# Kernel tuning notes

Measured on AMD Instinct MI355X. Metric: run time of the kernel, lower is better.

The kernel has to match this reference:

```python
import jax, jax.numpy as jnp
import numpy as np

B, T, D, H = 4, 2048, 1024, 16
HD = D // H  # head_size = 64
EPS = 1e-5


def layernorm(x, g, b):
    mu = jnp.mean(x, axis=-1, keepdims=True)
    var = jnp.var(x, axis=-1, keepdims=True)
    return (x - mu) * jax.lax.rsqrt(var + EPS) * g + b


def setup_inputs() -> dict:
    key = jax.random.key(0)
    ks = jax.random.split(key, 8)
    s = 0.02
    return {
        "x": jax.random.normal(ks[0], (B, T, D), jnp.float32),
        "Wq": jax.random.normal(ks[1], (D, D), jnp.float32) * s,
        "Wk": jax.random.normal(ks[2], (D, D), jnp.float32) * s,
        "Wv": jax.random.normal(ks[3], (D, D), jnp.float32) * s,
        "Wo": jax.random.normal(ks[4], (D, D), jnp.float32) * s,
        "bo": jnp.zeros((D,), jnp.float32),
        "W1": jax.random.normal(ks[5], (D, 4 * D), jnp.float32) * s,
        "b1": jnp.zeros((4 * D,), jnp.float32),
        "W2": jax.random.normal(ks[6], (4 * D, D), jnp.float32) * s,
        "b2": jnp.zeros((D,), jnp.float32),
        "ln1_g": jnp.ones((D,), jnp.float32),
        "ln1_b": jnp.zeros((D,), jnp.float32),
        "ln2_g": jnp.ones((D,), jnp.float32),
        "ln2_b": jnp.zeros((D,), jnp.float32),
    }


def reference(x, Wq, Wk, Wv, Wo, bo, W1, b1, W2, b2, ln1_g, ln1_b, ln2_g, ln2_b):
    # --- multi-head causal self-attention (pre-LN), dropout off (eval) ---
    h = layernorm(x, ln1_g, ln1_b)
    q = jnp.einsum('btd,de->bte', h, Wq).reshape(B, T, H, HD)
    k = jnp.einsum('btd,de->bte', h, Wk).reshape(B, T, H, HD)
    v = jnp.einsum('btd,de->bte', h, Wv).reshape(B, T, H, HD)
    scores = jnp.einsum('bqhd,bkhd->bhqk', q, k) * (HD ** -0.5)
    causal = jnp.tril(jnp.ones((T, T), bool))
    scores = jnp.where(causal, scores, -jnp.inf)
    attn = jax.nn.softmax(scores, axis=-1)
    out = jnp.einsum('bhqk,bkhd->bqhd', attn, v).reshape(B, T, D)
    out = jnp.einsum('btd,de->bte', out, Wo) + bo
    x = x + out
    # --- feed-forward: Linear -> ReLU -> Linear -> ReLU (as in source) ---
    h2 = layernorm(x, ln2_g, ln2_b)
    ff = jax.nn.relu(jnp.einsum('btd,df->btf', h2, W1) + b1)
    ff = jax.nn.relu(jnp.einsum('btf,fd->btd', ff, W2) + b2)
    return x + ff
```

## Files before the change

### kernel.cpp

```cpp
#include <hip/hip_runtime.h>
#include <cstdint>
#include <cstddef>

typedef unsigned short u16;
typedef __attribute__((ext_vector_type(8))) short bf16x8;
typedef __attribute__((ext_vector_type(4))) float f32x4;
typedef __attribute__((address_space(1))) const unsigned int gu32;
typedef __attribute__((address_space(3))) unsigned int lu32;

#define QSCALE 0.1803368801111204f

__device__ __forceinline__ u16 f2bf(float f) {
  uint32_t u = __float_as_uint(f);
  u += 0x7fffu + ((u >> 16) & 1u);
  return (u16)(u >> 16);
}

__device__ __forceinline__ void xcd_swz(int& bn, int& bm) {
  int gx = (int)gridDim.x;
  int n = gx * (int)gridDim.y;
  int lid = (int)blockIdx.x + gx * (int)blockIdx.y;
  int nid = (lid & 7) * (n >> 3) + (lid >> 3);
  bn = nid % gx;
  bm = nid / gx;
}

__global__ __launch_bounds__(256) void transpose_w(const float* __restrict__ W,
                                                   u16* __restrict__ WT,
                                                   int K, int N) {
  __shared__ float t[32][33];
  int n0 = blockIdx.x * 32, k0 = blockIdx.y * 32;
  for (int i = threadIdx.y; i < 32; i += 8)
    t[i][threadIdx.x] = W[(size_t)(k0 + i) * N + n0 + threadIdx.x];
  __syncthreads();
  for (int i = threadIdx.y; i < 32; i += 8)
    WT[(size_t)(n0 + i) * K + k0 + threadIdx.x] = f2bf(t[threadIdx.x][i]);
}

__global__ __launch_bounds__(256) void transpose_w4(
    const float* __restrict__ W0, const float* __restrict__ W1,
    const float* __restrict__ W2, const float* __restrict__ W3,
    u16* __restrict__ D0, u16* __restrict__ D1,
    u16* __restrict__ D2, u16* __restrict__ D3) {
  __shared__ float t[32][33];
  const float* W = (blockIdx.z == 0) ? W0 : (blockIdx.z == 1) ? W1
                   : (blockIdx.z == 2) ? W2 : W3;
  u16* D = (blockIdx.z == 0) ? D0 : (blockIdx.z == 1) ? D1
           : (blockIdx.z == 2) ? D2 : D3;
  int n0 = blockIdx.x * 32, k0 = blockIdx.y * 32;
  for (int i = threadIdx.y; i < 32; i += 8)
    t[i][threadIdx.x] = W[(size_t)(k0 + i) * 1024 + n0 + threadIdx.x];
  __syncthreads();
  for (int i = threadIdx.y; i < 32; i += 8)
    D[(size_t)(n0 + i) * 1024 + k0 + threadIdx.x] = f2bf(t[threadIdx.x][i]);
}

__global__ __launch_bounds__(256) void ln_kernel(const float* __restrict__ x,
                                                 const float* __restrict__ g,
                                                 const float* __restrict__ b,
                                                 u16* __restrict__ out) {
  int row = blockIdx.x;
  const float4 v = *(const float4*)(x + (size_t)row * 1024 + threadIdx.x * 4);
  float s = v.x + v.y + v.z + v.w;
  float ss = v.x * v.x + v.y * v.y + v.z * v.z + v.w * v.w;
#pragma unroll
  for (int d = 1; d < 64; d <<= 1) { s += __shfl_xor(s, d); ss += __shfl_xor(ss, d); }
  __shared__ float rs_[4], rss_[4];
  int wv = threadIdx.x >> 6;
  if ((threadIdx.x & 63) == 0) { rs_[wv] = s; rss_[wv] = ss; }
  __syncthreads();
  s = rs_[0] + rs_[1] + rs_[2] + rs_[3];
  ss = rss_[0] + rss_[1] + rss_[2] + rss_[3];
  float mu = s * (1.f / 1024.f);
  float var = ss * (1.f / 1024.f) - mu * mu;
  float rstd = rsqrtf(var + 1e-5f);
  float4 gv = *(const float4*)(g + threadIdx.x * 4);
  float4 bv = *(const float4*)(b + threadIdx.x * 4);
  uint32_t lo = (uint32_t)f2bf((v.x - mu) * rstd * gv.x + bv.x) |
                ((uint32_t)f2bf((v.y - mu) * rstd * gv.y + bv.y) << 16);
  uint32_t hi = (uint32_t)f2bf((v.z - mu) * rstd * gv.z + bv.z) |
                ((uint32_t)f2bf((v.w - mu) * rstd * gv.w + bv.w) << 16);
  uint2 o; o.x = lo; o.y = hi;
  *(uint2*)(out + (size_t)row * 1024 + threadIdx.x * 4) = o;
}

#define G128A(is)                                                             \
  __builtin_amdgcn_global_load_lds(                                           \
      (gu32*)((const char*)(A + (size_t)(bm * 128 + (is) * 32 + srow) * K +   \
                            (size_t)kt * 64) + ssw),                          \
      (lu32*)&lds[(is) * 2048 + wid * 512], 16, 0, 0)
#define G128B(is)                                                             \
  __builtin_amdgcn_global_load_lds(                                           \
      (gu32*)((const char*)(BT + (size_t)(bn * 128 + (is) * 32 + srow) * K +  \
                            (size_t)kt * 64) + ssw),                          \
      (lu32*)&lds[8192 + (is) * 2048 + wid * 512], 16, 0, 0)

template <int MODE>
__global__ __launch_bounds__(256, 4) void g128(
    const u16* __restrict__ A, const u16* __restrict__ BT,
    int M, int N, int K,
    const float* __restrict__ bias, const float* __restrict__ resid,
    float* __restrict__ outf,
    u16* __restrict__ ob0, u16* __restrict__ ob1, u16* __restrict__ ob2) {
  __shared__ __align__(16) u16 lds[16384];
  const int tid = threadIdx.x, lane = tid & 63, wid = tid >> 6;
  const int wr = wid >> 1, wc = wid & 1;
  int bn, bm;
  xcd_swz(bn, bm);
  const int l15 = lane & 15, lhi = lane >> 4;
  const int srow = tid >> 3;
  const int ssw = ((tid & 7) * 16) ^ ((srow & 7) << 4);
  const int swz = (l15 & 7) << 4;
  const int cb0 = (lhi * 16) ^ swz;
  const int cb1 = (64 + lhi * 16) ^ swz;
  const char* Ab = (const char*)lds;
  const char* Bb = (const char*)lds + 16384;

  f32x4 acc[4][4];
#pragma unroll
  for (int i = 0; i < 4; ++i)
#pragma unroll
    for (int j = 0; j < 4; ++j) acc[i][j] = (f32x4){0.f, 0.f, 0.f, 0.f};

  const int NT = K >> 6;

  for (int kt = 0; kt < NT; ++kt) {
    __syncthreads();
    G128A(0); G128A(1); G128A(2); G128A(3);
    G128B(0); G128B(1); G128B(2); G128B(3);
    __syncthreads();
#pragma unroll
    for (int ks = 0; ks < 2; ++ks) {
      const int cb = ks ? cb1 : cb0;
      bf16x8 af[4], bf[4];
#pragma unroll
      for (int mi = 0; mi < 4; ++mi)
        af[mi] = *(const bf16x8*)(Ab + (wr * 64 + mi * 16 + l15) * 128 + cb);
#pragma unroll
      for (int ni = 0; ni < 4; ++ni)
        bf[ni] = *(const bf16x8*)(Bb + (wc * 64 + ni * 16 + l15) * 128 + cb);
#pragma unroll
      for (int mi = 0; mi < 4; ++mi)
#pragma unroll
        for (int ni = 0; ni < 4; ++ni)
          acc[mi][ni] = __builtin_amdgcn_mfma_f32_16x16x32_bf16(af[mi], bf[ni], acc[mi][ni], 0, 0, 0);
    }
  }

  char* ep = (char*)lds;
  if (MODE == 0 && bn >= 16) {
#pragma unroll
    for (int h = 0; h < 2; ++h) {
      __syncthreads();
      if (wc == h) {
#pragma unroll
        for (int mi = 0; mi < 4; ++mi)
#pragma unroll
          for (int ni = 0; ni < 4; ++ni) {
            uint32_t lo, hi;
            asm("v_cvt_pk_bf16_f32 %0, %1, %2"
                : "=v"(lo) : "v"(acc[mi][ni][0]), "v"(acc[mi][ni][1]));
            asm("v_cvt_pk_bf16_f32 %0, %1, %2"
                : "=v"(hi) : "v"(acc[mi][ni][2]), "v"(acc[mi][ni][3]));
            uint2 pk; pk.x = lo; pk.y = hi;
            int c_local = ni * 16 + l15;
            int rb = wr * 64 + mi * 16 + lhi * 4;
            *(uint2*)(ep + c_local * 264 + rb * 2) = pk;
          }
      }
      __syncthreads();
#pragma unroll
      for (int it = 0; it < 4; ++it) {
        int idx = it * 256 + tid;
        int c = idx >> 4, tc = idx & 15;
        uint4 d4 = *(const uint4*)(ep + c * 264 + tc * 16);
        int cm = bn * 128 + h * 64 + c - 2048, hh = cm >> 6, dd = cm & 63;
        size_t bh = (size_t)((bm >> 4) * 16 + hh);
        int t0 = (bm & 15) * 128;
        *(uint4*)&ob2[(bh * 64 + dd) * 2048 + t0 + tc * 8] = d4;
      }
    }
  } else if (MODE == 0 || MODE == 2) {
    const float sc = (MODE == 0 && bn < 8) ? QSCALE : 1.f;
#pragma unroll
    for (int h = 0; h < 2; ++h) {
      __syncthreads();
      if (wr == h) {
#pragma unroll
        for (int mi = 0; mi < 4; ++mi)
#pragma unroll
          for (int ni = 0; ni < 4; ++ni) {
            int c_local = wc * 64 + ni * 16 + l15;
            int rb = mi * 16 + lhi * 4;
            float bv = (MODE == 2) ? bias[bn * 128 + c_local] : 0.f;
#pragma unroll
            for (int r = 0; r < 4; ++r) {
              float v = acc[mi][ni][r];
              v = (MODE == 2) ? fmaxf(v + bv, 0.f) : v * sc;
              *(u16*)(ep + (rb + r) * 272 + c_local * 2) = f2bf(v);
            }
          }
      }
      __syncthreads();
#pragma unroll
      for (int it = 0; it < 4; ++it) {
        int idx = it * 256 + tid;
        int row = idx >> 4, cc = idx & 15;
        uint4 d4 = *(const uint4*)(ep + row * 272 + cc * 16);
        size_t rg = (size_t)(bm * 128 + h * 64 + row);
        int colg = bn * 128 + cc * 8;
        if (MODE == 2) {
          *(uint4*)&ob0[rg * (size_t)N + colg] = d4;
        } else if (colg < 1024) {
          *(uint4*)&ob0[rg * 1024 + colg] = d4;
        } else {
          *(uint4*)&ob1[rg * 1024 + colg - 1024] = d4;
        }
      }
    }
  } else {
    float* epf = (float*)lds;
#pragma unroll
    for (int q = 0; q < 4; ++q) {
      __syncthreads();
      if (wr == (q >> 1)) {
#pragma unroll
        for (int mh = 0; mh < 2; ++mh) {
          int mi = (q & 1) * 2 + mh;
#pragma unroll
          for (int ni = 0; ni < 4; ++ni) {
            int c_local = wc * 64 + ni * 16 + l15;
            int rl = mh * 16 + lhi * 4;
#pragma unroll
            for (int r = 0; r < 4; ++r)
              epf[(rl + r) * 132 + c_local] = acc[mi][ni][r];
          }
        }
      }
      __syncthreads();
#pragma unroll
      for (int it = 0; it < 4; ++it) {
        int idx = it * 256 + tid;
        int row = idx >> 5, cc = idx & 31;
        float4 v = *(const float4*)&epf[row * 132 + cc * 4];
        int colg = bn * 128 + cc * 4;
        size_t rg = (size_t)(bm * 128 + q * 32 + row);
        float4 bv = *(const float4*)&bias[colg];
        float4 rv = *(const float4*)&resid[rg * (size_t)N + colg];
        float4 o4;
        if (MODE == 1) {
          o4.x = v.x + bv.x + rv.x; o4.y = v.y + bv.y + rv.y;
          o4.z = v.z + bv.z + rv.z; o4.w = v.w + bv.w + rv.w;
        } else {
          o4.x = fmaxf(v.x + bv.x, 0.f) + rv.x;
          o4.y = fmaxf(v.y + bv.y, 0.f) + rv.y;
          o4.z = fmaxf(v.z + bv.z, 0.f) + rv.z;
          o4.w = fmaxf(v.w + bv.w, 0.f) + rv.w;
        }
        *(float4*)&outf[rg * (size_t)N + colg] = o4;
      }
    }
  }
}

__global__ __launch_bounds__(512) void attn_kernel(
    const u16* __restrict__ Qb, const u16* __restrict__ Kb,
    const u16* __restrict__ VTb, u16* __restrict__ O) {
  const int lid = (int)blockIdx.x + 8 * (int)blockIdx.y;
  const int p = (lid >> 3) & 7;
  const int bh = ((lid >> 6) << 3) | (lid & 7);
  const int b = bh >> 4, h = bh & 15;
  const u16* Q = Qb + (size_t)b * 2048 * 1024 + h * 64;
  const u16* Kn = Kb + (size_t)b * 2048 * 1024 + h * 64;
  const u16* VT = VTb + (size_t)bh * 64 * 2048;
  const int tid = threadIdx.x, lane = tid & 63, wv = tid >> 6;
  const int l15 = lane & 15, lhi = lane >> 4;
  const int srow = tid >> 3;
  const int scol16 = (tid & 7) * 16;
  const int sw = scol16 ^ ((srow & 7) << 4);
  const int rswz = (l15 & 7) << 4;
  const int cb0 = (lhi * 16) ^ rswz;
  const int cb1 = (64 + lhi * 16) ^ rswz;

  __shared__ __align__(16) u16 KV[3][2][4096];
  __shared__ u16 Ps[8][16 * 72];

  bf16x8 onesf;
#pragma unroll
  for (int i = 0; i < 8; ++i) onesf[i] = (short)0x3F80;

#define STAGEKV(slot, kt)                                                     \
  do {                                                                        \
    __builtin_amdgcn_global_load_lds(                                         \
        (gu32*)((const char*)(Kn + (size_t)((kt)*64 + srow) * 1024) + sw),    \
        (lu32*)&KV[slot][0][wv * 512], 16, 0, 0);                             \
    __builtin_amdgcn_global_load_lds(                                         \
        (gu32*)((const char*)(VT + (size_t)srow * 2048 + (kt)*64) + sw),      \
        (lu32*)&KV[slot][1][wv * 512], 16, 0, 0);                             \
  } while (0)

#pragma unroll
  for (int pass = 0; pass < 2; ++pass) {
    const int chunk = pass ? p : (15 - p);
    const int qbase = chunk * 128 + wv * 16;
    const int nkt = 2 * chunk + 2;

    bf16x8 qf[2];
#pragma unroll
    for (int ks = 0; ks < 2; ++ks)
      qf[ks] = *(const bf16x8*)&Q[(size_t)(qbase + l15) * 1024 + ks * 32 + lhi * 8];

    f32x4 o[4];
#pragma unroll
    for (int f = 0; f < 4; ++f) o[f] = (f32x4){0.f, 0.f, 0.f, 0.f};
    f32x4 lacc = (f32x4){0.f, 0.f, 0.f, 0.f};

    __syncthreads();
    STAGEKV(0, 0);
    STAGEKV(1, 1);

    for (int kt = 0; kt < nkt; ++kt) {
      if (kt + 1 < nkt) {
        asm volatile("s_waitcnt vmcnt(2)" ::: "memory");
      } else {
        asm volatile("s_waitcnt vmcnt(0)" ::: "memory");
      }
      __syncthreads();

      const int cs = kt % 3;
      if (kt * 64 <= qbase + 15) {
        const char* Kbase = (const char*)&KV[cs][0][0];
        const char* Vbase = (const char*)&KV[cs][1][0];

        f32x4 s[4];
#pragma unroll
        for (int jt = 0; jt < 4; ++jt) s[jt] = (f32x4){0.f, 0.f, 0.f, 0.f};
        __builtin_amdgcn_s_setprio(1);
#pragma unroll
        for (int ks = 0; ks < 2; ++ks) {
          const int cbyte = ks ? cb1 : cb0;
#pragma unroll
          for (int jt = 0; jt < 4; ++jt) {
            bf16x8 kf = *(const bf16x8*)(Kbase + (jt * 16 + l15) * 128 + cbyte);
            s[jt] = __builtin_amdgcn_mfma_f32_16x16x32_bf16(kf, qf[ks], s[jt], 0, 0, 0);
          }
        }
        __builtin_amdgcn_s_setprio(0);

        if (kt * 64 + 63 > qbase) {
          int qg = qbase + l15;
#pragma unroll
          for (int jt = 0; jt < 4; ++jt)
#pragma unroll
            for (int r = 0; r < 4; ++r) {
              int kg = kt * 64 + jt * 16 + lhi * 4 + r;
              if (kg > qg) s[jt][r] = -1e30f;
            }
        }

#pragma unroll
        for (int jt = 0; jt < 4; ++jt)
#pragma unroll
          for (int r = 0; r < 4; ++r) s[jt][r] = exp2f(s[jt][r]);

#pragma unroll
        for (int jt = 0; jt < 4; ++jt) {
          uint32_t lo, hi;
          asm("v_cvt_pk_bf16_f32 %0, %1, %2"
              : "=v"(lo) : "v"(s[jt][0]), "v"(s[jt][1]));
          asm("v_cvt_pk_bf16_f32 %0, %1, %2"
              : "=v"(hi) : "v"(s[jt][2]), "v"(s[jt][3]));
          uint2 pk; pk.x = lo; pk.y = hi;
          *(uint2*)&Ps[wv][l15 * 72 + jt * 16 + lhi * 4] = pk;
        }
        __builtin_amdgcn_s_setprio(1);
#pragma unroll
        for (int ks = 0; ks < 2; ++ks) {
          const int cbyte = ks ? cb1 : cb0;
          bf16x8 pf = *(const bf16x8*)&Ps[wv][l15 * 72 + ks * 32 + lhi * 8];
          lacc = __builtin_amdgcn_mfma_f32_16x16x32_bf16(pf, onesf, lacc, 0, 0, 0);
#pragma unroll
          for (int f = 0; f < 4; ++f) {
            bf16x8 vfr = *(const bf16x8*)(Vbase + (f * 16 + l15) * 128 + cbyte);
            o[f] = __builtin_amdgcn_mfma_f32_16x16x32_bf16(pf, vfr, o[f], 0, 0, 0);
          }
        }
        __builtin_amdgcn_s_setprio(0);
      }

      if (kt + 2 < nkt) STAGEKV((kt + 2) % 3, kt + 2);
    }

#pragma unroll
    for (int r = 0; r < 4; ++r) {
      float inv = 1.f / lacc[r];
      int t = qbase + lhi * 4 + r;
#pragma unroll
      for (int f = 0; f < 4; ++f)
        O[((size_t)(b * 2048 + t)) * 1024 + h * 64 + f * 16 + l15] = f2bf(o[f][r] * inv);
    }
  }
#undef STAGEKV
}

extern "C" void kernel_launch(void* const* d_in, const int* in_sizes, int n_in,
                              void* d_out, int out_size, void* d_ws, size_t ws_size,
                              hipStream_t stream) {
  const float* x   = (const float*)d_in[0];
  const float* Wq  = (const float*)d_in[1];
  const float* Wk  = (const float*)d_in[2];
  const float* Wv  = (const float*)d_in[3];
  const float* Wo  = (const float*)d_in[4];
  const float* bo  = (const float*)d_in[5];
  const float* W1  = (const float*)d_in[6];
  const float* b1  = (const float*)d_in[7];
  const float* W2  = (const float*)d_in[8];
  const float* b2  = (const float*)d_in[9];
  const float* g1  = (const float*)d_in[10];
  const float* be1 = (const float*)d_in[11];
  const float* g2  = (const float*)d_in[12];
  const float* be2 = (const float*)d_in[13];

  char* p = (char*)d_ws;
  auto alloc = [&](size_t bytes) {
    char* r = p;
    p += (bytes + 255) & ~(size_t)255;
    return r;
  };
  u16* WqkvT = (u16*)alloc(3072ull * 1024 * 2);
  u16* WoT   = (u16*)alloc(1024ull * 1024 * 2);
  u16* W1T   = (u16*)alloc(4096ull * 1024 * 2);
  u16* W2T   = (u16*)alloc(1024ull * 4096 * 2);
  u16* hln   = (u16*)alloc(8192ull * 1024 * 2);
  u16* Qbuf  = (u16*)alloc(8192ull * 1024 * 2);
  u16* Kbuf  = (u16*)alloc(8192ull * 1024 * 2);
  u16* VTbuf = (u16*)alloc(8192ull * 1024 * 2);
  float* x2  = (float*)alloc(8192ull * 1024 * 4);
  u16* ff1   = (u16*)alloc(8192ull * 4096 * 2);
  u16* Oattn = hln;
  u16* h2    = Qbuf;
  if ((size_t)(p - (char*)d_ws) > ws_size) return;

  dim3 tb(32, 8);
  transpose_w4<<<dim3(32, 32, 4), tb, 0, stream>>>(
      Wq, Wk, Wv, Wo, WqkvT, WqkvT + 1024 * 1024, WqkvT + 2048 * 1024, WoT);
  transpose_w<<<dim3(128, 32), tb, 0, stream>>>(W1, W1T, 1024, 4096);
  transpose_w<<<dim3(32, 128), tb, 0, stream>>>(W2, W2T, 4096, 1024);

  ln_kernel<<<8192, 256, 0, stream>>>(x, g1, be1, hln);

  g128<0><<<dim3(24, 64), 256, 0, stream>>>(hln, WqkvT, 8192, 3072, 1024,
                                            nullptr, nullptr, nullptr,
                                            Qbuf, Kbuf, VTbuf);

  attn_kernel<<<dim3(8, 64), 512, 0, stream>>>(Qbuf, Kbuf, VTbuf, Oattn);

  g128<1><<<dim3(8, 64), 256, 0, stream>>>(Oattn, WoT, 8192, 1024, 1024,
                                           bo, x, x2, nullptr, nullptr, nullptr);

  ln_kernel<<<8192, 256, 0, stream>>>(x2, g2, be2, h2);

  g128<2><<<dim3(32, 64), 256, 0, stream>>>(h2, W1T, 8192, 4096, 1024,
                                            b1, nullptr, nullptr, ff1, nullptr, nullptr);

  g128<3><<<dim3(8, 64), 256, 0, stream>>>(ff1, W2T, 8192, 1024, 4096,
                                           b2, x2, (float*)d_out, nullptr, nullptr, nullptr);
}
```

Measured before the change: 364.4 us.

## Double-buffer LDS tiles in GEMM for small-grid output projections

Adds a PIPE template parameter to the 128x128 GEMM. When it is set, the kernel prefetches the next K-tile into a second LDS buffer while computing on the current one, and raises wave priority around the MFMA block. This is enabled for the Wo and W2 projections, whose 512-block grids leave the load latency exposed. It doubles LDS per block to 64KB and lowers launch bounds to 2 waves per SIMD for all variants, which may change register allocation and occupancy for the non-pipelined QKV and W1 GEMMs too.

```diff
diff --git a/kernel.cpp b/kernel.cpp
--- a/kernel.cpp
+++ b/kernel.cpp
@@ -84,25 +84,30 @@
   *(uint2*)(out + (size_t)row * 1024 + threadIdx.x * 4) = o;
 }
 
-#define G128A(is)                                                             \
+#define G128A(buf, t, is)                                                     \
   __builtin_amdgcn_global_load_lds(                                           \
       (gu32*)((const char*)(A + (size_t)(bm * 128 + (is) * 32 + srow) * K +   \
-                            (size_t)kt * 64) + ssw),                          \
-      (lu32*)&lds[(is) * 2048 + wid * 512], 16, 0, 0)
-#define G128B(is)                                                             \
+                            (size_t)(t) * 64) + ssw),                         \
+      (lu32*)&lds[(buf) * 16384 + (is) * 2048 + wid * 512], 16, 0, 0)
+#define G128B(buf, t, is)                                                     \
   __builtin_amdgcn_global_load_lds(                                           \
       (gu32*)((const char*)(BT + (size_t)(bn * 128 + (is) * 32 + srow) * K +  \
-                            (size_t)kt * 64) + ssw),                          \
-      (lu32*)&lds[8192 + (is) * 2048 + wid * 512], 16, 0, 0)
-
-template <int MODE>
-__global__ __launch_bounds__(256, 4) void g128(
+                            (size_t)(t) * 64) + ssw),                         \
+      (lu32*)&lds[(buf) * 16384 + 8192 + (is) * 2048 + wid * 512], 16, 0, 0)
+#define STAGE128(buf, t)                                                      \
+  do {                                                                        \
+    G128A(buf, t, 0); G128A(buf, t, 1); G128A(buf, t, 2); G128A(buf, t, 3);   \
+    G128B(buf, t, 0); G128B(buf, t, 1); G128B(buf, t, 2); G128B(buf, t, 3);   \
+  } while (0)
+
+template <int MODE, int PIPE>
+__global__ __launch_bounds__(256, 2) void g128(
     const u16* __restrict__ A, const u16* __restrict__ BT,
     int M, int N, int K,
     const float* __restrict__ bias, const float* __restrict__ resid,
     float* __restrict__ outf,
     u16* __restrict__ ob0, u16* __restrict__ ob1, u16* __restrict__ ob2) {
-  __shared__ __align__(16) u16 lds[16384];
+  __shared__ __align__(16) u16 lds[PIPE ? 32768 : 16384];
   const int tid = threadIdx.x, lane = tid & 63, wid = tid >> 6;
   const int wr = wid >> 1, wc = wid & 1;
   int bn, bm;
@@ -113,8 +118,6 @@
   const int swz = (l15 & 7) << 4;
   const int cb0 = (lhi * 16) ^ swz;
   const int cb1 = (64 + lhi * 16) ^ swz;
-  const char* Ab = (const char*)lds;
-  const char* Bb = (const char*)lds + 16384;
 
   f32x4 acc[4][4];
 #pragma unroll
@@ -124,26 +127,57 @@
 
   const int NT = K >> 6;
 
-  for (int kt = 0; kt < NT; ++kt) {
-    __syncthreads();
-    G128A(0); G128A(1); G128A(2); G128A(3);
-    G128B(0); G128B(1); G128B(2); G128B(3);
-    __syncthreads();
-#pragma unroll
-    for (int ks = 0; ks < 2; ++ks) {
-      const int cb = ks ? cb1 : cb0;
-      bf16x8 af[4], bf[4];
-#pragma unroll
-      for (int mi = 0; mi < 4; ++mi)
-        af[mi] = *(const bf16x8*)(Ab + (wr * 64 + mi * 16 + l15) * 128 + cb);
-#pragma unroll
-      for (int ni = 0; ni < 4; ++ni)
-        bf[ni] = *(const bf16x8*)(Bb + (wc * 64 + ni * 16 + l15) * 128 + cb);
-#pragma unroll
-      for (int mi = 0; mi < 4; ++mi)
+  if (PIPE) {
+    STAGE128(0, 0);
+    for (int kt = 0; kt < NT; ++kt) {
+      const int buf = kt & 1;
+      asm volatile("s_waitcnt vmcnt(0)" ::: "memory");
+      __syncthreads();
+      if (kt + 1 < NT) STAGE128(buf ^ 1, kt + 1);
+      const char* Ab = (const char*)lds + buf * 32768;
+      const char* Bb = Ab + 16384;
+#pragma unroll
+      for (int ks = 0; ks < 2; ++ks) {
+        const int cb = ks ? cb1 : cb0;
+        bf16x8 af[4], bf[4];
+#pragma unroll
+        for (int mi = 0; mi < 4; ++mi)
+          af[mi] = *(const bf16x8*)(Ab + (wr * 64 + mi * 16 + l15) * 128 + cb);
 #pragma unroll
         for (int ni = 0; ni < 4; ++ni)
-          acc[mi][ni] = __builtin_amdgcn_mfma_f32_16x16x32_bf16(af[mi], bf[ni], acc[mi][ni], 0, 0, 0);
+          bf[ni] = *(const bf16x8*)(Bb + (wc * 64 + ni * 16 + l15) * 128 + cb);
+        __builtin_amdgcn_s_setprio(1);
+#pragma unroll
+        for (int mi = 0; mi < 4; ++mi)
+#pragma unroll
+          for (int ni = 0; ni < 4; ++ni)
+            acc[mi][ni] = __builtin_amdgcn_mfma_f32_16x16x32_bf16(af[mi], bf[ni], acc[mi][ni], 0, 0, 0);
+        __builtin_amdgcn_s_setprio(0);
+      }
+    }
+  } else {
+    for (int kt = 0; kt < NT; ++kt) {
+      __syncthreads();
+      STAGE128(0, kt);
+      __syncthreads();
+      const char* Ab = (const char*)lds;
+      const char* Bb = Ab + 16384;
+#pragma unroll
+      for (int ks = 0; ks < 2; ++ks) {
+        const int cb = ks ? cb1 : cb0;
+        bf16x8 af[4], bf[4];
+#pragma unroll
+        for (int mi = 0; mi < 4; ++mi)
+          af[mi] = *(const bf16x8*)(Ab + (wr * 64 + mi * 16 + l15) * 128 + cb);
+#pragma unroll
+        for (int ni = 0; ni < 4; ++ni)
+          bf[ni] = *(const bf16x8*)(Bb + (wc * 64 + ni * 16 + l15) * 128 + cb);
+#pragma unroll
+        for (int mi = 0; mi < 4; ++mi)
+#pragma unroll
+          for (int ni = 0; ni < 4; ++ni)
+            acc[mi][ni] = __builtin_amdgcn_mfma_f32_16x16x32_bf16(af[mi], bf[ni], acc[mi][ni], 0, 0, 0);
+      }
     }
   }
 
@@ -449,20 +483,20 @@
 
   ln_kernel<<<8192, 256, 0, stream>>>(x, g1, be1, hln);
 
-  g128<0><<<dim3(24, 64), 256, 0, stream>>>(hln, WqkvT, 8192, 3072, 1024,
-                                            nullptr, nullptr, nullptr,
-                                            Qbuf, Kbuf, VTbuf);
+  g128<0, 0><<<dim3(24, 64), 256, 0, stream>>>(hln, WqkvT, 8192, 3072, 1024,
+                                               nullptr, nullptr, nullptr,
+                                               Qbuf, Kbuf, VTbuf);
 
   attn_kernel<<<dim3(8, 64), 512, 0, stream>>>(Qbuf, Kbuf, VTbuf, Oattn);
 
-  g128<1><<<dim3(8, 64), 256, 0, stream>>>(Oattn, WoT, 8192, 1024, 1024,
-                                           bo, x, x2, nullptr, nullptr, nullptr);
+  g128<1, 1><<<dim3(8, 64), 256, 0, stream>>>(Oattn, WoT, 8192, 1024, 1024,
+                                              bo, x, x2, nullptr, nullptr, nullptr);
 
   ln_kernel<<<8192, 256, 0, stream>>>(x2, g2, be2, h2);
 
-  g128<2><<<dim3(32, 64), 256, 0, stream>>>(h2, W1T, 8192, 4096, 1024,
-                                            b1, nullptr, nullptr, ff1, nullptr, nullptr);
-
-  g128<3><<<dim3(8, 64), 256, 0, stream>>>(ff1, W2T, 8192, 1024, 4096,
-                                           b2, x2, (float*)d_out, nullptr, nullptr, nullptr);
-}
+  g128<2, 0><<<dim3(32, 64), 256, 0, stream>>>(h2, W1T, 8192, 4096, 1024,
+                                               b1, nullptr, nullptr, ff1, nullptr, nullptr);
+
+  g128<3, 1><<<dim3(8, 64), 256, 0, stream>>>(ff1, W2T, 8192, 1024, 4096,
+                                              b2, x2, (float*)d_out, nullptr, nullptr, nullptr);
+}
```

Result: faster. 348.4 us, median of 2 (-4.4%).
